# Optimization experiments

Hardware: AMD Instinct MI355X
Metric: run time of the kernel (lower is better)

Reference implementation:

```python
import jax, jax.numpy as jnp
import numpy as np

SIGMA = 1.0
TOP_K = 4

def setup_inputs() -> dict:
    key = jax.random.key(0)
    k1, k2, k3, k4 = jax.random.split(key, 4)
    B, N, IN_DIM, OUT_DIM, P = 2, 4096, 128, 128, 3
    x = jax.random.normal(k1, (B, N, IN_DIM), dtype=jnp.float32)
    pos = jax.random.normal(k2, (B, N, P), dtype=jnp.float32)
    # Linear(in_dim, out_dim): W [in_dim, out_dim], b [out_dim]
    lim = 1.0 / np.sqrt(IN_DIM)
    W = jax.random.uniform(k3, (IN_DIM, OUT_DIM), minval=-lim, maxval=lim, dtype=jnp.float32)
    b = jax.random.uniform(k4, (OUT_DIM,), minval=-lim, maxval=lim, dtype=jnp.float32)
    return {"x": x, "pos": pos, "W": W, "b": b}

def reference(x, pos, W, b):
    B, N, _ = x.shape
    # pairwise distances [B, N, N]
    pos_diff = pos[:, :, None, :] - pos[:, None, :, :]
    dist = jnp.sqrt(jnp.sum(pos_diff ** 2, axis=-1) + 1e-8)
    adj = jnp.exp(-dist ** 2 / (2.0 * SIGMA ** 2))
    # top-k mask along last dim
    _, indices = jax.lax.top_k(adj, TOP_K)  # [B, N, k]
    b_idx = jnp.arange(B)[:, None, None]
    n_idx = jnp.arange(N)[None, :, None]
    mask = jnp.zeros_like(adj).at[b_idx, n_idx, indices].set(1.0)
    adj = adj * mask
    adj = adj / (jnp.sum(adj, axis=-1, keepdims=True) + 1e-8)
    # weighted aggregation + linear
    out = jnp.einsum('bnm,bmd->bnd', adj, x)
    return out @ W + b
```

## Files before the change

kernel.cpp:

```cpp
#include <hip/hip_runtime.h>
#include <hip/hip_bf16.h>

#define NPTS 4096
#define NROWS 8192
#define DIM 128
#define GEMM_BLOCKS 1024
#define HCELL 0.25f
#define LOW (-4.0f)
#define CAP 16
#define NCELLS 32768
#define OVCAP 4096

typedef __attribute__((ext_vector_type(8))) short bf16x8;
typedef __attribute__((ext_vector_type(4))) float f32x4;

__device__ __forceinline__ int cellcoord(float v) {
    int c = (int)floorf((v - LOW) / HCELL);
    return c < 0 ? 0 : (c > 31 ? 31 : c);
}

__global__ __launch_bounds__(256) void k1_gemm_bin(const float* __restrict__ x,
        const float* __restrict__ pos, const float* __restrict__ W,
        __hip_bfloat16* __restrict__ xWb, unsigned* __restrict__ cellCnt,
        float4* __restrict__ cellPts, unsigned* __restrict__ ovfCnt,
        float4* __restrict__ ovfList) {
    int b = blockIdx.x;
    if (b >= GEMM_BLOCKS) {
        int t = (b - GEMM_BLOCKS) * 256 + threadIdx.x;
        int batch = t >> 12;
        const float* p = pos + (size_t)t * 3;
        float px = p[0], py = p[1], pz = p[2];
        int cx = cellcoord(px), cy = cellcoord(py), cz = cellcoord(pz);
        int cid = ((batch * 32 + cz) * 32 + cy) * 32 + cx;
        unsigned slot = atomicAdd(&cellCnt[cid], 1u);
        float4 rec = make_float4(px, py, pz, __uint_as_float((unsigned)(t & (NPTS - 1))));
        if (slot < CAP) cellPts[(size_t)cid * CAP + slot] = rec;
        else { unsigned o = atomicAdd(&ovfCnt[batch], 1u);
               if (o < OVCAP) ovfList[(size_t)batch * OVCAP + o] = rec; }
        return;
    }
    int wave = threadIdx.x >> 6, lane = threadIdx.x & 63;
    int tile = b * 4 + wave;
    int m0 = (tile >> 3) << 4, n0 = (tile & 7) << 4;
    int r = lane & 15, kg = lane >> 4;
    const float* xr = x + (size_t)(m0 + r) * DIM + kg * 8;
    const float* wc = W + (size_t)(kg * 8) * DIM + (n0 + r);
    f32x4 acc = {0.f, 0.f, 0.f, 0.f};
    union { __hip_bfloat16 h; short s; } u;
#pragma unroll
    for (int kb = 0; kb < 4; ++kb) {
        float4 a0 = *(const float4*)(xr + kb * 32);
        float4 a1 = *(const float4*)(xr + kb * 32 + 4);
        bf16x8 af, bf;
        u.h = __float2bfloat16(a0.x); af[0] = u.s;
        u.h = __float2bfloat16(a0.y); af[1] = u.s;
        u.h = __float2bfloat16(a0.z); af[2] = u.s;
        u.h = __float2bfloat16(a0.w); af[3] = u.s;
        u.h = __float2bfloat16(a1.x); af[4] = u.s;
        u.h = __float2bfloat16(a1.y); af[5] = u.s;
        u.h = __float2bfloat16(a1.z); af[6] = u.s;
        u.h = __float2bfloat16(a1.w); af[7] = u.s;
#pragma unroll
        for (int i = 0; i < 8; ++i) {
            u.h = __float2bfloat16(wc[(size_t)(kb * 32 + i) * DIM]);
            bf[i] = u.s;
        }
        acc = __builtin_amdgcn_mfma_f32_16x16x32_bf16(af, bf, acc, 0, 0, 0);
    }
    int col = n0 + r, rbase = m0 + (kg << 2);
#pragma unroll
    for (int reg = 0; reg < 4; ++reg)
        xWb[(size_t)(rbase + reg) * DIM + col] = __float2bfloat16(acc[reg]);
}

__device__ __forceinline__ double mkkey(float d2, int j) {
    return __longlong_as_double(__double_as_longlong((double)d2) |
                                (unsigned long long)(unsigned)j);
}
__device__ __forceinline__ void kins(double& k0, double& k1, double& k2,
                                     double& k3, double s) {
    double c = fmax(k0, s); k0 = fmin(k0, s);
    double t = fmax(k1, c); k1 = fmin(k1, c); c = t;
    t = fmax(k2, c);        k2 = fmin(k2, c); c = t;
    k3 = fmin(k3, c);
}
__device__ __forceinline__ void kmerge(double& a0, double& a1, double& a2,
                                       double& a3, double b0, double b1,
                                       double b2, double b3) {
    double m0 = fmin(a0, b3), m1 = fmin(a1, b2);
    double m2 = fmin(a2, b1), m3 = fmin(a3, b0);
    double t0 = fmin(m0, m2), t2 = fmax(m0, m2);
    double t1 = fmin(m1, m3), t3 = fmax(m1, m3);
    a0 = fmin(t0, t1); a1 = fmax(t0, t1);
    a2 = fmin(t2, t3); a3 = fmax(t2, t3);
}

__global__ __launch_bounds__(256) void knn_agg(const unsigned* __restrict__ cellCnt,
        const float4* __restrict__ cellPts, const unsigned* __restrict__ ovfCnt,
        const float4* __restrict__ ovfList, const float* __restrict__ pos,
        const __hip_bfloat16* __restrict__ xWb, const float* __restrict__ bias,
        float* __restrict__ out) {
    int lane = threadIdx.x & 63;
    int wave = threadIdx.x >> 6;
    int row = blockIdx.x * 4 + wave;
    int batch = row >> 12;
    int qi = row & (NPTS - 1);
    const float* pb = pos + (size_t)batch * NPTS * 3;
    float qx = pb[3 * qi], qy = pb[3 * qi + 1], qz = pb[3 * qi + 2];
    int cx = cellcoord(qx), cy = cellcoord(qy), cz = cellcoord(qz);
    const unsigned* cb = cellCnt + (size_t)batch * NCELLS;
    const float4* pb4 = cellPts + (size_t)batch * NCELLS * CAP;

    const double INF = __builtin_inf();
    double k0 = INF, k1 = INF, k2 = INF, k3 = INF;

#pragma unroll
    for (int mm = 0; mm < 2; ++mm) {
        int m = lane + mm * 64;
        if (m < 125) {
            int dz = m / 25 - 2, dy = (m / 5) % 5 - 2, dx = m % 5 - 2;
            int nx = cx + dx, ny = cy + dy, nz = cz + dz;
            if ((unsigned)nx < 32u && (unsigned)ny < 32u && (unsigned)nz < 32u) {
                int lid = (nz * 32 + ny) * 32 + nx;
                unsigned c = cb[lid]; c = c < CAP ? c : CAP;
                const float4* cp = pb4 + (size_t)lid * CAP;
                for (unsigned s = 0; s < c; ++s) {
                    float4 p = cp[s];
                    float ddx = qx - p.x, ddy = qy - p.y, ddz = qz - p.z;
                    float d2 = fmaf(ddx, ddx, fmaf(ddy, ddy, ddz * ddz));
                    kins(k0, k1, k2, k3, mkkey(d2, (int)__float_as_uint(p.w)));
                }
            }
        }
    }
#pragma unroll
    for (int off = 1; off < 64; off <<= 1) {
        double p0 = __shfl_xor(k0, off), p1 = __shfl_xor(k1, off);
        double p2 = __shfl_xor(k2, off), p3 = __shfl_xor(k3, off);
        kmerge(k0, k1, k2, k3, p0, p1, p2, p3);
    }

    float dbox = 1e30f;
    if (cx - 2 > 0)  dbox = fminf(dbox, qx - (LOW + (cx - 2) * HCELL));
    if (cx + 2 < 31) dbox = fminf(dbox, (LOW + (cx + 3) * HCELL) - qx);
    if (cy - 2 > 0)  dbox = fminf(dbox, qy - (LOW + (cy - 2) * HCELL));
    if (cy + 2 < 31) dbox = fminf(dbox, (LOW + (cy + 3) * HCELL) - qy);
    if (cz - 2 > 0)  dbox = fminf(dbox, qz - (LOW + (cz - 2) * HCELL));
    if (cz + 2 < 31) dbox = fminf(dbox, (LOW + (cz + 3) * HCELL) - qz);
    bool resolved = ((float)k3 < 0.999f * dbox * dbox) && ((float)k3 < 1e29f);

    if (!resolved) {
        k0 = INF; k1 = INF; k2 = INF; k3 = INF;
#pragma unroll 4
        for (int t = 0; t < NPTS / 64; ++t) {
            int j = t * 64 + lane;
            float px = pb[3 * j], py = pb[3 * j + 1], pz = pb[3 * j + 2];
            float ddx = qx - px, ddy = qy - py, ddz = qz - pz;
            float d2 = fmaf(ddx, ddx, fmaf(ddy, ddy, ddz * ddz));
            kins(k0, k1, k2, k3, mkkey(d2, j));
        }
#pragma unroll
        for (int off = 1; off < 64; off <<= 1) {
            double p0 = __shfl_xor(k0, off), p1 = __shfl_xor(k1, off);
            double p2 = __shfl_xor(k2, off), p3 = __shfl_xor(k3, off);
            kmerge(k0, k1, k2, k3, p0, p1, p2, p3);
        }
    } else {
        unsigned oc = ovfCnt[batch]; oc = oc < OVCAP ? oc : OVCAP;
        const float4* ol = ovfList + (size_t)batch * OVCAP;
        for (unsigned o = 0; o < oc; ++o) {
            float4 p = ol[o];
            float ddx = qx - p.x, ddy = qy - p.y, ddz = qz - p.z;
            float d2 = fmaf(ddx, ddx, fmaf(ddy, ddy, ddz * ddz));
            kins(k0, k1, k2, k3, mkkey(d2, (int)__float_as_uint(p.w)));
        }
    }

    unsigned i0 = (unsigned)__double_as_longlong(k0) & 0xFFFu;
    unsigned i1 = (unsigned)__double_as_longlong(k1) & 0xFFFu;
    unsigned i2 = (unsigned)__double_as_longlong(k2) & 0xFFFu;
    unsigned i3 = (unsigned)__double_as_longlong(k3) & 0xFFFu;
    float d0 = (float)k0, d1 = (float)k1, d2 = (float)k2, d3 = (float)k3;
    float w0 = __expf(-(d0 + 1e-8f) * 0.5f);
    float w1 = __expf(-(d1 + 1e-8f) * 0.5f);
    float w2 = __expf(-(d2 + 1e-8f) * 0.5f);
    float w3 = __expf(-(d3 + 1e-8f) * 0.5f);
    float inv = 1.0f / (w0 + w1 + w2 + w3 + 1e-8f);
    w0 *= inv; w1 *= inv; w2 *= inv; w3 *= inv;
    int c = lane << 1;
    float2 bb = *(const float2*)(bias + c);
    const unsigned short* xu = (const unsigned short*)xWb;
    size_t bbase = ((size_t)batch * NPTS) << 7;
    ushort2 g0 = *(const ushort2*)(xu + bbase + ((size_t)i0 << 7) + c);
    ushort2 g1 = *(const ushort2*)(xu + bbase + ((size_t)i1 << 7) + c);
    ushort2 g2 = *(const ushort2*)(xu + bbase + ((size_t)i2 << 7) + c);
    ushort2 g3 = *(const ushort2*)(xu + bbase + ((size_t)i3 << 7) + c);
    float ox = bb.x + w0 * __uint_as_float((unsigned)g0.x << 16)
                    + w1 * __uint_as_float((unsigned)g1.x << 16)
                    + w2 * __uint_as_float((unsigned)g2.x << 16)
                    + w3 * __uint_as_float((unsigned)g3.x << 16);
    float oy = bb.y + w0 * __uint_as_float((unsigned)g0.y << 16)
                    + w1 * __uint_as_float((unsigned)g1.y << 16)
                    + w2 * __uint_as_float((unsigned)g2.y << 16)
                    + w3 * __uint_as_float((unsigned)g3.y << 16);
    *(float2*)(out + ((size_t)row << 7) + c) = make_float2(ox, oy);
}

extern "C" void kernel_launch(void* const* d_in, const int* in_sizes, int n_in,
                              void* d_out, int out_size, void* d_ws, size_t ws_size,
                              hipStream_t stream) {
    const float* x    = (const float*)d_in[0];
    const float* pos  = (const float*)d_in[1];
    const float* W    = (const float*)d_in[2];
    const float* bias = (const float*)d_in[3];
    float* out = (float*)d_out;

    char* ws = (char*)d_ws;
    __hip_bfloat16* xWb = (__hip_bfloat16*)ws;
    unsigned* cellCnt  = (unsigned*)(ws + 2097152);
    unsigned* ovfCnt   = (unsigned*)(ws + 2359296);
    float4* cellPts    = (float4*)(ws + 2359312);
    float4* ovfList    = (float4*)(ws + 2359312 + 16777216);

    hipMemsetAsync(ws + 2097152, 0, 262160, stream);
    k1_gemm_bin<<<GEMM_BLOCKS + NROWS / 256, 256, 0, stream>>>(
        x, pos, W, xWb, cellCnt, cellPts, ovfCnt, ovfList);
    knn_agg<<<NROWS / 4, 256, 0, stream>>>(
        cellCnt, cellPts, ovfCnt, ovfList, pos, xWb, bias, out);
}
```

Measured before the change: 84.27 us.

## Fuse memset, GEMM/binning and kNN aggregation into one cooperative kernel

Replaces the memset plus two kernel launches with a single cooperative kernel of 1024 blocks. It clears the cell counters, runs the GEMM tiles and point binning, and then each wave handles two kNN rows, with grid-wide syncs between the phases. This is meant to remove launch gaps and the separate memset. The cost is two grid barriers and fewer concurrent waves for the kNN phase. The old multi-kernel path is kept as a fallback if the cooperative launch fails.

```diff
diff --git a/kernel.cpp b/kernel.cpp
--- a/kernel.cpp
+++ b/kernel.cpp
@@ -1,5 +1,8 @@
 #include <hip/hip_runtime.h>
 #include <hip/hip_bf16.h>
+#include <hip/hip_cooperative_groups.h>
+
+namespace cg = cooperative_groups;
 
 #define NPTS 4096
 #define NROWS 8192
@@ -19,28 +22,40 @@
     return c < 0 ? 0 : (c > 31 ? 31 : c);
 }
 
-__global__ __launch_bounds__(256) void k1_gemm_bin(const float* __restrict__ x,
-        const float* __restrict__ pos, const float* __restrict__ W,
-        __hip_bfloat16* __restrict__ xWb, unsigned* __restrict__ cellCnt,
-        float4* __restrict__ cellPts, unsigned* __restrict__ ovfCnt,
-        float4* __restrict__ ovfList) {
-    int b = blockIdx.x;
-    if (b >= GEMM_BLOCKS) {
-        int t = (b - GEMM_BLOCKS) * 256 + threadIdx.x;
-        int batch = t >> 12;
-        const float* p = pos + (size_t)t * 3;
-        float px = p[0], py = p[1], pz = p[2];
-        int cx = cellcoord(px), cy = cellcoord(py), cz = cellcoord(pz);
-        int cid = ((batch * 32 + cz) * 32 + cy) * 32 + cx;
-        unsigned slot = atomicAdd(&cellCnt[cid], 1u);
-        float4 rec = make_float4(px, py, pz, __uint_as_float((unsigned)(t & (NPTS - 1))));
-        if (slot < CAP) cellPts[(size_t)cid * CAP + slot] = rec;
-        else { unsigned o = atomicAdd(&ovfCnt[batch], 1u);
-               if (o < OVCAP) ovfList[(size_t)batch * OVCAP + o] = rec; }
-        return;
-    }
-    int wave = threadIdx.x >> 6, lane = threadIdx.x & 63;
-    int tile = b * 4 + wave;
+__device__ __forceinline__ double mkkey(float d2, int j) {
+    return __longlong_as_double(__double_as_longlong((double)d2) |
+                                (unsigned long long)(unsigned)j);
+}
+__device__ __forceinline__ void kins(double& k0, double& k1, double& k2,
+                                     double& k3, double s) {
+    double c = fmax(k0, s); k0 = fmin(k0, s);
+    double t = fmax(k1, c); k1 = fmin(k1, c); c = t;
+    t = fmax(k2, c);        k2 = fmin(k2, c); c = t;
+    k3 = fmin(k3, c);
+}
+__device__ __forceinline__ void kmerge(double& a0, double& a1, double& a2,
+                                       double& a3, double b0, double b1,
+                                       double b2, double b3) {
+    double m0 = fmin(a0, b3), m1 = fmin(a1, b2);
+    double m2 = fmin(a2, b1), m3 = fmin(a3, b0);
+    double t0 = fmin(m0, m2), t2 = fmax(m0, m2);
+    double t1 = fmin(m1, m3), t3 = fmax(m1, m3);
+    a0 = fmin(t0, t1); a1 = fmax(t0, t1);
+    a2 = fmin(t2, t3); a3 = fmax(t2, t3);
+}
+__device__ __forceinline__ void wave_bfly(double& k0, double& k1,
+                                          double& k2, double& k3) {
+#pragma unroll
+    for (int off = 1; off < 64; off <<= 1) {
+        double p0 = __shfl_xor(k0, off), p1 = __shfl_xor(k1, off);
+        double p2 = __shfl_xor(k2, off), p3 = __shfl_xor(k3, off);
+        kmerge(k0, k1, k2, k3, p0, p1, p2, p3);
+    }
+}
+
+__device__ __forceinline__ void gemm_tile_body(const float* __restrict__ x,
+        const float* __restrict__ W, __hip_bfloat16* __restrict__ xWb,
+        int tile, int lane) {
     int m0 = (tile >> 3) << 4, n0 = (tile & 7) << 4;
     int r = lane & 15, kg = lane >> 4;
     const float* xr = x + (size_t)(m0 + r) * DIM + kg * 8;
@@ -73,36 +88,26 @@
         xWb[(size_t)(rbase + reg) * DIM + col] = __float2bfloat16(acc[reg]);
 }
 
-__device__ __forceinline__ double mkkey(float d2, int j) {
-    return __longlong_as_double(__double_as_longlong((double)d2) |
-                                (unsigned long long)(unsigned)j);
-}
-__device__ __forceinline__ void kins(double& k0, double& k1, double& k2,
-                                     double& k3, double s) {
-    double c = fmax(k0, s); k0 = fmin(k0, s);
-    double t = fmax(k1, c); k1 = fmin(k1, c); c = t;
-    t = fmax(k2, c);        k2 = fmin(k2, c); c = t;
-    k3 = fmin(k3, c);
-}
-__device__ __forceinline__ void kmerge(double& a0, double& a1, double& a2,
-                                       double& a3, double b0, double b1,
-                                       double b2, double b3) {
-    double m0 = fmin(a0, b3), m1 = fmin(a1, b2);
-    double m2 = fmin(a2, b1), m3 = fmin(a3, b0);
-    double t0 = fmin(m0, m2), t2 = fmax(m0, m2);
-    double t1 = fmin(m1, m3), t3 = fmax(m1, m3);
-    a0 = fmin(t0, t1); a1 = fmax(t0, t1);
-    a2 = fmin(t2, t3); a3 = fmax(t2, t3);
-}
-
-__global__ __launch_bounds__(256) void knn_agg(const unsigned* __restrict__ cellCnt,
+__device__ __forceinline__ void bin_point_body(const float* __restrict__ pos,
+        unsigned* __restrict__ cellCnt, float4* __restrict__ cellPts,
+        unsigned* __restrict__ ovfCnt, float4* __restrict__ ovfList, int t) {
+    int batch = t >> 12;
+    const float* p = pos + (size_t)t * 3;
+    float px = p[0], py = p[1], pz = p[2];
+    int cx = cellcoord(px), cy = cellcoord(py), cz = cellcoord(pz);
+    int cid = ((batch * 32 + cz) * 32 + cy) * 32 + cx;
+    unsigned slot = atomicAdd(&cellCnt[cid], 1u);
+    float4 rec = make_float4(px, py, pz, __uint_as_float((unsigned)(t & (NPTS - 1))));
+    if (slot < CAP) cellPts[(size_t)cid * CAP + slot] = rec;
+    else { unsigned o = atomicAdd(&ovfCnt[batch], 1u);
+           if (o < OVCAP) ovfList[(size_t)batch * OVCAP + o] = rec; }
+}
+
+__device__ __forceinline__ void knn_row_body(const unsigned* __restrict__ cellCnt,
         const float4* __restrict__ cellPts, const unsigned* __restrict__ ovfCnt,
         const float4* __restrict__ ovfList, const float* __restrict__ pos,
         const __hip_bfloat16* __restrict__ xWb, const float* __restrict__ bias,
-        float* __restrict__ out) {
-    int lane = threadIdx.x & 63;
-    int wave = threadIdx.x >> 6;
-    int row = blockIdx.x * 4 + wave;
+        float* __restrict__ out, int row, int lane) {
     int batch = row >> 12;
     int qi = row & (NPTS - 1);
     const float* pb = pos + (size_t)batch * NPTS * 3;
@@ -133,12 +138,7 @@
             }
         }
     }
-#pragma unroll
-    for (int off = 1; off < 64; off <<= 1) {
-        double p0 = __shfl_xor(k0, off), p1 = __shfl_xor(k1, off);
-        double p2 = __shfl_xor(k2, off), p3 = __shfl_xor(k3, off);
-        kmerge(k0, k1, k2, k3, p0, p1, p2, p3);
-    }
+    wave_bfly(k0, k1, k2, k3);
 
     float dbox = 1e30f;
     if (cx - 2 > 0)  dbox = fminf(dbox, qx - (LOW + (cx - 2) * HCELL));
@@ -159,12 +159,7 @@
             float d2 = fmaf(ddx, ddx, fmaf(ddy, ddy, ddz * ddz));
             kins(k0, k1, k2, k3, mkkey(d2, j));
         }
-#pragma unroll
-        for (int off = 1; off < 64; off <<= 1) {
-            double p0 = __shfl_xor(k0, off), p1 = __shfl_xor(k1, off);
-            double p2 = __shfl_xor(k2, off), p3 = __shfl_xor(k3, off);
-            kmerge(k0, k1, k2, k3, p0, p1, p2, p3);
-        }
+        wave_bfly(k0, k1, k2, k3);
     } else {
         unsigned oc = ovfCnt[batch]; oc = oc < OVCAP ? oc : OVCAP;
         const float4* ol = ovfList + (size_t)batch * OVCAP;
@@ -206,6 +201,56 @@
     *(float2*)(out + ((size_t)row << 7) + c) = make_float2(ox, oy);
 }
 
+__global__ __launch_bounds__(256, 4) void fused(const float* __restrict__ x,
+        const float* __restrict__ pos, const float* __restrict__ W,
+        const float* __restrict__ bias, __hip_bfloat16* __restrict__ xWb,
+        unsigned* __restrict__ cellCnt, float4* __restrict__ cellPts,
+        unsigned* __restrict__ ovfCnt, float4* __restrict__ ovfList,
+        float* __restrict__ out) {
+    cg::grid_group gg = cg::this_grid();
+    int bid = blockIdx.x, tid = threadIdx.x;
+    int wave = tid >> 6, lane = tid & 63;
+
+    {
+        int idx = bid * 256 + tid;
+        if (idx < 2 * NCELLS + 2) cellCnt[idx] = 0;
+    }
+    gg.sync();
+
+    gemm_tile_body(x, W, xWb, bid * 4 + wave, lane);
+    if (tid < 8) bin_point_body(pos, cellCnt, cellPts, ovfCnt, ovfList,
+                                bid * 8 + tid);
+    gg.sync();
+
+#pragma unroll 1
+    for (int rep = 0; rep < 2; ++rep)
+        knn_row_body(cellCnt, cellPts, ovfCnt, ovfList, pos, xWb, bias, out,
+                     bid * 8 + wave * 2 + rep, lane);
+}
+
+__global__ __launch_bounds__(256) void k1_gemm_bin(const float* __restrict__ x,
+        const float* __restrict__ pos, const float* __restrict__ W,
+        __hip_bfloat16* __restrict__ xWb, unsigned* __restrict__ cellCnt,
+        float4* __restrict__ cellPts, unsigned* __restrict__ ovfCnt,
+        float4* __restrict__ ovfList) {
+    int b = blockIdx.x;
+    if (b >= GEMM_BLOCKS) {
+        bin_point_body(pos, cellCnt, cellPts, ovfCnt, ovfList,
+                       (b - GEMM_BLOCKS) * 256 + threadIdx.x);
+        return;
+    }
+    gemm_tile_body(x, W, xWb, b * 4 + (threadIdx.x >> 6), threadIdx.x & 63);
+}
+
+__global__ __launch_bounds__(256) void knn_agg(const unsigned* __restrict__ cellCnt,
+        const float4* __restrict__ cellPts, const unsigned* __restrict__ ovfCnt,
+        const float4* __restrict__ ovfList, const float* __restrict__ pos,
+        const __hip_bfloat16* __restrict__ xWb, const float* __restrict__ bias,
+        float* __restrict__ out) {
+    knn_row_body(cellCnt, cellPts, ovfCnt, ovfList, pos, xWb, bias, out,
+                 blockIdx.x * 4 + (threadIdx.x >> 6), threadIdx.x & 63);
+}
+
 extern "C" void kernel_launch(void* const* d_in, const int* in_sizes, int n_in,
                               void* d_out, int out_size, void* d_ws, size_t ws_size,
                               hipStream_t stream) {
@@ -222,9 +267,16 @@
     float4* cellPts    = (float4*)(ws + 2359312);
     float4* ovfList    = (float4*)(ws + 2359312 + 16777216);
 
-    hipMemsetAsync(ws + 2097152, 0, 262160, stream);
-    k1_gemm_bin<<<GEMM_BLOCKS + NROWS / 256, 256, 0, stream>>>(
-        x, pos, W, xWb, cellCnt, cellPts, ovfCnt, ovfList);
-    knn_agg<<<NROWS / 4, 256, 0, stream>>>(
-        cellCnt, cellPts, ovfCnt, ovfList, pos, xWb, bias, out);
-}
+    void* args[10] = { (void*)&x, (void*)&pos, (void*)&W, (void*)&bias,
+                       (void*)&xWb, (void*)&cellCnt, (void*)&cellPts,
+                       (void*)&ovfCnt, (void*)&ovfList, (void*)&out };
+    hipError_t e = hipLaunchCooperativeKernel((const void*)fused, dim3(1024),
+                                              dim3(256), args, 0, stream);
+    if (e != hipSuccess) {
+        hipMemsetAsync(ws + 2097152, 0, 262160, stream);
+        k1_gemm_bin<<<GEMM_BLOCKS + NROWS / 256, 256, 0, stream>>>(
+            x, pos, W, xWb, cellCnt, cellPts, ovfCnt, ovfList);
+        knn_agg<<<NROWS / 4, 256, 0, stream>>>(
+            cellCnt, cellPts, ovfCnt, ovfList, pos, xWb, bias, out);
+    }
+}
```

Result: slower. 253.4 us (+200.6%).

## Process two query rows per wave in kNN aggregation kernel

Applied to the files above, without the earlier changes.

Each wavefront now handles two consecutive query rows, interleaving their cell scans in one loop and merging both top-4 lists in the same shuffle reduction. The grid is halved to match. The aim is more instruction-level parallelism and memory-latency hiding per wave, plus amortising the shuffle-merge overhead. In exchange it raises register pressure (eight double keys), adds divergence when the two rows have different cell counts, and halves the number of waves in flight.

```diff
diff --git a/kernel.cpp b/kernel.cpp
--- a/kernel.cpp
+++ b/kernel.cpp
@@ -102,108 +102,201 @@
         float* __restrict__ out) {
     int lane = threadIdx.x & 63;
     int wave = threadIdx.x >> 6;
-    int row = blockIdx.x * 4 + wave;
-    int batch = row >> 12;
-    int qi = row & (NPTS - 1);
-    const float* pb = pos + (size_t)batch * NPTS * 3;
-    float qx = pb[3 * qi], qy = pb[3 * qi + 1], qz = pb[3 * qi + 2];
-    int cx = cellcoord(qx), cy = cellcoord(qy), cz = cellcoord(qz);
-    const unsigned* cb = cellCnt + (size_t)batch * NCELLS;
-    const float4* pb4 = cellPts + (size_t)batch * NCELLS * CAP;
+    int pairI = blockIdx.x * 4 + wave;
+    int rA = pairI * 2, rB = rA + 1;
+    int batA = rA >> 12, batB = rB >> 12;
+    int qiA = rA & (NPTS - 1), qiB = rB & (NPTS - 1);
+    const float* pbA = pos + (size_t)batA * NPTS * 3;
+    const float* pbB = pos + (size_t)batB * NPTS * 3;
+    float qxA = pbA[3 * qiA], qyA = pbA[3 * qiA + 1], qzA = pbA[3 * qiA + 2];
+    float qxB = pbB[3 * qiB], qyB = pbB[3 * qiB + 1], qzB = pbB[3 * qiB + 2];
+    int cxA = cellcoord(qxA), cyA = cellcoord(qyA), czA = cellcoord(qzA);
+    int cxB = cellcoord(qxB), cyB = cellcoord(qyB), czB = cellcoord(qzB);
+    const unsigned* cbA = cellCnt + (size_t)batA * NCELLS;
+    const unsigned* cbB = cellCnt + (size_t)batB * NCELLS;
+    const float4* p4A = cellPts + (size_t)batA * NCELLS * CAP;
+    const float4* p4B = cellPts + (size_t)batB * NCELLS * CAP;
 
     const double INF = __builtin_inf();
-    double k0 = INF, k1 = INF, k2 = INF, k3 = INF;
+    double a0 = INF, a1 = INF, a2 = INF, a3 = INF;
+    double b0 = INF, b1 = INF, b2 = INF, b3 = INF;
 
 #pragma unroll
     for (int mm = 0; mm < 2; ++mm) {
         int m = lane + mm * 64;
+        int nA = 0, nB = 0;
+        const float4* cpA = p4A;
+        const float4* cpB = p4B;
         if (m < 125) {
             int dz = m / 25 - 2, dy = (m / 5) % 5 - 2, dx = m % 5 - 2;
-            int nx = cx + dx, ny = cy + dy, nz = cz + dz;
+            int nx = cxA + dx, ny = cyA + dy, nz = czA + dz;
             if ((unsigned)nx < 32u && (unsigned)ny < 32u && (unsigned)nz < 32u) {
                 int lid = (nz * 32 + ny) * 32 + nx;
-                unsigned c = cb[lid]; c = c < CAP ? c : CAP;
-                const float4* cp = pb4 + (size_t)lid * CAP;
-                for (unsigned s = 0; s < c; ++s) {
-                    float4 p = cp[s];
-                    float ddx = qx - p.x, ddy = qy - p.y, ddz = qz - p.z;
-                    float d2 = fmaf(ddx, ddx, fmaf(ddy, ddy, ddz * ddz));
-                    kins(k0, k1, k2, k3, mkkey(d2, (int)__float_as_uint(p.w)));
-                }
+                int c = (int)cbA[lid]; nA = c < CAP ? c : CAP;
+                cpA = p4A + (size_t)lid * CAP;
             }
+            nx = cxB + dx; ny = cyB + dy; nz = czB + dz;
+            if ((unsigned)nx < 32u && (unsigned)ny < 32u && (unsigned)nz < 32u) {
+                int lid = (nz * 32 + ny) * 32 + nx;
+                int c = (int)cbB[lid]; nB = c < CAP ? c : CAP;
+                cpB = p4B + (size_t)lid * CAP;
+            }
+        }
+        int n = nA > nB ? nA : nB;
+        for (int s = 0; s < n; ++s) {
+            if (s < nA) {
+                float4 p = cpA[s];
+                float ddx = qxA - p.x, ddy = qyA - p.y, ddz = qzA - p.z;
+                float d2 = fmaf(ddx, ddx, fmaf(ddy, ddy, ddz * ddz));
+                kins(a0, a1, a2, a3, mkkey(d2, (int)__float_as_uint(p.w)));
+            }
+            if (s < nB) {
+                float4 p = cpB[s];
+                float ddx = qxB - p.x, ddy = qyB - p.y, ddz = qzB - p.z;
+                float d2 = fmaf(ddx, ddx, fmaf(ddy, ddy, ddz * ddz));
+                kins(b0, b1, b2, b3, mkkey(d2, (int)__float_as_uint(p.w)));
+            }
         }
     }
 #pragma unroll
     for (int off = 1; off < 64; off <<= 1) {
-        double p0 = __shfl_xor(k0, off), p1 = __shfl_xor(k1, off);
-        double p2 = __shfl_xor(k2, off), p3 = __shfl_xor(k3, off);
-        kmerge(k0, k1, k2, k3, p0, p1, p2, p3);
-    }
-
-    float dbox = 1e30f;
-    if (cx - 2 > 0)  dbox = fminf(dbox, qx - (LOW + (cx - 2) * HCELL));
-    if (cx + 2 < 31) dbox = fminf(dbox, (LOW + (cx + 3) * HCELL) - qx);
-    if (cy - 2 > 0)  dbox = fminf(dbox, qy - (LOW + (cy - 2) * HCELL));
-    if (cy + 2 < 31) dbox = fminf(dbox, (LOW + (cy + 3) * HCELL) - qy);
-    if (cz - 2 > 0)  dbox = fminf(dbox, qz - (LOW + (cz - 2) * HCELL));
-    if (cz + 2 < 31) dbox = fminf(dbox, (LOW + (cz + 3) * HCELL) - qz);
-    bool resolved = ((float)k3 < 0.999f * dbox * dbox) && ((float)k3 < 1e29f);
-
-    if (!resolved) {
-        k0 = INF; k1 = INF; k2 = INF; k3 = INF;
+        double pa0 = __shfl_xor(a0, off), pa1 = __shfl_xor(a1, off);
+        double pa2 = __shfl_xor(a2, off), pa3 = __shfl_xor(a3, off);
+        double pb0 = __shfl_xor(b0, off), pb1 = __shfl_xor(b1, off);
+        double pb2 = __shfl_xor(b2, off), pb3 = __shfl_xor(b3, off);
+        kmerge(a0, a1, a2, a3, pa0, pa1, pa2, pa3);
+        kmerge(b0, b1, b2, b3, pb0, pb1, pb2, pb3);
+    }
+
+    float dbA = 1e30f;
+    if (cxA - 2 > 0)  dbA = fminf(dbA, qxA - (LOW + (cxA - 2) * HCELL));
+    if (cxA + 2 < 31) dbA = fminf(dbA, (LOW + (cxA + 3) * HCELL) - qxA);
+    if (cyA - 2 > 0)  dbA = fminf(dbA, qyA - (LOW + (cyA - 2) * HCELL));
+    if (cyA + 2 < 31) dbA = fminf(dbA, (LOW + (cyA + 3) * HCELL) - qyA);
+    if (czA - 2 > 0)  dbA = fminf(dbA, qzA - (LOW + (czA - 2) * HCELL));
+    if (czA + 2 < 31) dbA = fminf(dbA, (LOW + (czA + 3) * HCELL) - qzA);
+    bool resA = ((float)a3 < 0.999f * dbA * dbA) && ((float)a3 < 1e29f);
+
+    float dbB = 1e30f;
+    if (cxB - 2 > 0)  dbB = fminf(dbB, qxB - (LOW + (cxB - 2) * HCELL));
+    if (cxB + 2 < 31) dbB = fminf(dbB, (LOW + (cxB + 3) * HCELL) - qxB);
+    if (cyB - 2 > 0)  dbB = fminf(dbB, qyB - (LOW + (cyB - 2) * HCELL));
+    if (cyB + 2 < 31) dbB = fminf(dbB, (LOW + (cyB + 3) * HCELL) - qyB);
+    if (czB - 2 > 0)  dbB = fminf(dbB, qzB - (LOW + (czB - 2) * HCELL));
+    if (czB + 2 < 31) dbB = fminf(dbB, (LOW + (czB + 3) * HCELL) - qzB);
+    bool resB = ((float)b3 < 0.999f * dbB * dbB) && ((float)b3 < 1e29f);
+
+    if (!resA) {
+        a0 = INF; a1 = INF; a2 = INF; a3 = INF;
 #pragma unroll 4
         for (int t = 0; t < NPTS / 64; ++t) {
             int j = t * 64 + lane;
-            float px = pb[3 * j], py = pb[3 * j + 1], pz = pb[3 * j + 2];
-            float ddx = qx - px, ddy = qy - py, ddz = qz - pz;
+            float px = pbA[3 * j], py = pbA[3 * j + 1], pz = pbA[3 * j + 2];
+            float ddx = qxA - px, ddy = qyA - py, ddz = qzA - pz;
             float d2 = fmaf(ddx, ddx, fmaf(ddy, ddy, ddz * ddz));
-            kins(k0, k1, k2, k3, mkkey(d2, j));
+            kins(a0, a1, a2, a3, mkkey(d2, j));
         }
 #pragma unroll
         for (int off = 1; off < 64; off <<= 1) {
-            double p0 = __shfl_xor(k0, off), p1 = __shfl_xor(k1, off);
-            double p2 = __shfl_xor(k2, off), p3 = __shfl_xor(k3, off);
-            kmerge(k0, k1, k2, k3, p0, p1, p2, p3);
+            double p0 = __shfl_xor(a0, off), p1 = __shfl_xor(a1, off);
+            double p2 = __shfl_xor(a2, off), p3 = __shfl_xor(a3, off);
+            kmerge(a0, a1, a2, a3, p0, p1, p2, p3);
         }
     } else {
-        unsigned oc = ovfCnt[batch]; oc = oc < OVCAP ? oc : OVCAP;
-        const float4* ol = ovfList + (size_t)batch * OVCAP;
+        unsigned oc = ovfCnt[batA]; oc = oc < OVCAP ? oc : OVCAP;
+        const float4* ol = ovfList + (size_t)batA * OVCAP;
         for (unsigned o = 0; o < oc; ++o) {
             float4 p = ol[o];
-            float ddx = qx - p.x, ddy = qy - p.y, ddz = qz - p.z;
+            float ddx = qxA - p.x, ddy = qyA - p.y, ddz = qzA - p.z;
             float d2 = fmaf(ddx, ddx, fmaf(ddy, ddy, ddz * ddz));
-            kins(k0, k1, k2, k3, mkkey(d2, (int)__float_as_uint(p.w)));
-        }
-    }
-
-    unsigned i0 = (unsigned)__double_as_longlong(k0) & 0xFFFu;
-    unsigned i1 = (unsigned)__double_as_longlong(k1) & 0xFFFu;
-    unsigned i2 = (unsigned)__double_as_longlong(k2) & 0xFFFu;
-    unsigned i3 = (unsigned)__double_as_longlong(k3) & 0xFFFu;
-    float d0 = (float)k0, d1 = (float)k1, d2 = (float)k2, d3 = (float)k3;
-    float w0 = __expf(-(d0 + 1e-8f) * 0.5f);
-    float w1 = __expf(-(d1 + 1e-8f) * 0.5f);
-    float w2 = __expf(-(d2 + 1e-8f) * 0.5f);
-    float w3 = __expf(-(d3 + 1e-8f) * 0.5f);
-    float inv = 1.0f / (w0 + w1 + w2 + w3 + 1e-8f);
-    w0 *= inv; w1 *= inv; w2 *= inv; w3 *= inv;
+            kins(a0, a1, a2, a3, mkkey(d2, (int)__float_as_uint(p.w)));
+        }
+    }
+
+    if (!resB) {
+        b0 = INF; b1 = INF; b2 = INF; b3 = INF;
+#pragma unroll 4
+        for (int t = 0; t < NPTS / 64; ++t) {
+            int j = t * 64 + lane;
+            float px = pbB[3 * j], py = pbB[3 * j + 1], pz = pbB[3 * j + 2];
+            float ddx = qxB - px, ddy = qyB - py, ddz = qzB - pz;
+            float d2 = fmaf(ddx, ddx, fmaf(ddy, ddy, ddz * ddz));
+            kins(b0, b1, b2, b3, mkkey(d2, j));
+        }
+#pragma unroll
+        for (int off = 1; off < 64; off <<= 1) {
+            double p0 = __shfl_xor(b0, off), p1 = __shfl_xor(b1, off);
+            double p2 = __shfl_xor(b2, off), p3 = __shfl_xor(b3, off);
+            kmerge(b0, b1, b2, b3, p0, p1, p2, p3);
+        }
+    } else {
+        unsigned oc = ovfCnt[batB]; oc = oc < OVCAP ? oc : OVCAP;
+        const float4* ol = ovfList + (size_t)batB * OVCAP;
+        for (unsigned o = 0; o < oc; ++o) {
+            float4 p = ol[o];
+            float ddx = qxB - p.x, ddy = qyB - p.y, ddz = qzB - p.z;
+            float d2 = fmaf(ddx, ddx, fmaf(ddy, ddy, ddz * ddz));
+            kins(b0, b1, b2, b3, mkkey(d2, (int)__float_as_uint(p.w)));
+        }
+    }
+
     int c = lane << 1;
     float2 bb = *(const float2*)(bias + c);
     const unsigned short* xu = (const unsigned short*)xWb;
-    size_t bbase = ((size_t)batch * NPTS) << 7;
-    ushort2 g0 = *(const ushort2*)(xu + bbase + ((size_t)i0 << 7) + c);
-    ushort2 g1 = *(const ushort2*)(xu + bbase + ((size_t)i1 << 7) + c);
-    ushort2 g2 = *(const ushort2*)(xu + bbase + ((size_t)i2 << 7) + c);
-    ushort2 g3 = *(const ushort2*)(xu + bbase + ((size_t)i3 << 7) + c);
-    float ox = bb.x + w0 * __uint_as_float((unsigned)g0.x << 16)
-                    + w1 * __uint_as_float((unsigned)g1.x << 16)
-                    + w2 * __uint_as_float((unsigned)g2.x << 16)
-                    + w3 * __uint_as_float((unsigned)g3.x << 16);
-    float oy = bb.y + w0 * __uint_as_float((unsigned)g0.y << 16)
-                    + w1 * __uint_as_float((unsigned)g1.y << 16)
-                    + w2 * __uint_as_float((unsigned)g2.y << 16)
-                    + w3 * __uint_as_float((unsigned)g3.y << 16);
-    *(float2*)(out + ((size_t)row << 7) + c) = make_float2(ox, oy);
+    {
+        unsigned i0 = (unsigned)__double_as_longlong(a0) & 0xFFFu;
+        unsigned i1 = (unsigned)__double_as_longlong(a1) & 0xFFFu;
+        unsigned i2 = (unsigned)__double_as_longlong(a2) & 0xFFFu;
+        unsigned i3 = (unsigned)__double_as_longlong(a3) & 0xFFFu;
+        float d0 = (float)a0, d1 = (float)a1, d2 = (float)a2, d3 = (float)a3;
+        float w0 = __expf(-(d0 + 1e-8f) * 0.5f);
+        float w1 = __expf(-(d1 + 1e-8f) * 0.5f);
+        float w2 = __expf(-(d2 + 1e-8f) * 0.5f);
+        float w3 = __expf(-(d3 + 1e-8f) * 0.5f);
+        float inv = 1.0f / (w0 + w1 + w2 + w3 + 1e-8f);
+        w0 *= inv; w1 *= inv; w2 *= inv; w3 *= inv;
+        size_t bbase = ((size_t)batA * NPTS) << 7;
+        ushort2 g0 = *(const ushort2*)(xu + bbase + ((size_t)i0 << 7) + c);
+        ushort2 g1 = *(const ushort2*)(xu + bbase + ((size_t)i1 << 7) + c);
+        ushort2 g2 = *(const ushort2*)(xu + bbase + ((size_t)i2 << 7) + c);
+        ushort2 g3 = *(const ushort2*)(xu + bbase + ((size_t)i3 << 7) + c);
+        float ox = bb.x + w0 * __uint_as_float((unsigned)g0.x << 16)
+                        + w1 * __uint_as_float((unsigned)g1.x << 16)
+                        + w2 * __uint_as_float((unsigned)g2.x << 16)
+                        + w3 * __uint_as_float((unsigned)g3.x << 16);
+        float oy = bb.y + w0 * __uint_as_float((unsigned)g0.y << 16)
+                        + w1 * __uint_as_float((unsigned)g1.y << 16)
+                        + w2 * __uint_as_float((unsigned)g2.y << 16)
+                        + w3 * __uint_as_float((unsigned)g3.y << 16);
+        *(float2*)(out + ((size_t)rA << 7) + c) = make_float2(ox, oy);
+    }
+    {
+        unsigned i0 = (unsigned)__double_as_longlong(b0) & 0xFFFu;
+        unsigned i1 = (unsigned)__double_as_longlong(b1) & 0xFFFu;
+        unsigned i2 = (unsigned)__double_as_longlong(b2) & 0xFFFu;
+        unsigned i3 = (unsigned)__double_as_longlong(b3) & 0xFFFu;
+        float d0 = (float)b0, d1 = (float)b1, d2 = (float)b2, d3 = (float)b3;
+        float w0 = __expf(-(d0 + 1e-8f) * 0.5f);
+        float w1 = __expf(-(d1 + 1e-8f) * 0.5f);
+        float w2 = __expf(-(d2 + 1e-8f) * 0.5f);
+        float w3 = __expf(-(d3 + 1e-8f) * 0.5f);
+        float inv = 1.0f / (w0 + w1 + w2 + w3 + 1e-8f);
+        w0 *= inv; w1 *= inv; w2 *= inv; w3 *= inv;
+        size_t bbase = ((size_t)batB * NPTS) << 7;
+        ushort2 g0 = *(const ushort2*)(xu + bbase + ((size_t)i0 << 7) + c);
+        ushort2 g1 = *(const ushort2*)(xu + bbase + ((size_t)i1 << 7) + c);
+        ushort2 g2 = *(const ushort2*)(xu + bbase + ((size_t)i2 << 7) + c);
+        ushort2 g3 = *(const ushort2*)(xu + bbase + ((size_t)i3 << 7) + c);
+        float ox = bb.x + w0 * __uint_as_float((unsigned)g0.x << 16)
+                        + w1 * __uint_as_float((unsigned)g1.x << 16)
+                        + w2 * __uint_as_float((unsigned)g2.x << 16)
+                        + w3 * __uint_as_float((unsigned)g3.x << 16);
+        float oy = bb.y + w0 * __uint_as_float((unsigned)g0.y << 16)
+                        + w1 * __uint_as_float((unsigned)g1.y << 16)
+                        + w2 * __uint_as_float((unsigned)g2.y << 16)
+                        + w3 * __uint_as_float((unsigned)g3.y << 16);
+        *(float2*)(out + ((size_t)rB << 7) + c) = make_float2(ox, oy);
+    }
 }
 
 extern "C" void kernel_launch(void* const* d_in, const int* in_sizes, int n_in,
@@ -225,6 +318,6 @@
     hipMemsetAsync(ws + 2097152, 0, 262160, stream);
     k1_gemm_bin<<<GEMM_BLOCKS + NROWS / 256, 256, 0, stream>>>(
         x, pos, W, xWb, cellCnt, cellPts, ovfCnt, ovfList);
-    knn_agg<<<NROWS / 4, 256, 0, stream>>>(
+    knn_agg<<<NROWS / 8, 256, 0, stream>>>(
         cellCnt, cellPts, ovfCnt, ovfList, pos, xWb, bias, out);
 }
```

Result: slower. 88.85 us (+5.4%).
